# Kernel optimization log

Measured on AMD Instinct MI355X. Metric: run time of the kernel, lower is better.

## Reference

```python
import jax, jax.numpy as jnp
import numpy as np

B, N, D = 4, 2048, 1024
H, DH = 16, 64
SCALE = DH ** -0.5


def setup_inputs() -> dict:
    key = jax.random.key(0)
    k1, k2, k3 = jax.random.split(key, 3)
    z = jax.random.normal(k1, (B, N, D), dtype=jnp.float32)
    w_qkv = jax.random.normal(k2, (D, 3 * H * DH), dtype=jnp.float32) * (D ** -0.5)
    w_out = jax.random.normal(k3, (H * DH, D), dtype=jnp.float32) * ((H * DH) ** -0.5)
    b_out = jnp.zeros((D,), dtype=jnp.float32)
    return {"z": z, "w_qkv": w_qkv, "w_out": w_out, "b_out": b_out}


def reference(z, w_qkv, w_out, b_out):
    # qkv projection: (B,N,D) @ (D,3*H*DH) -> split into q,k,v
    qkv = z @ w_qkv  # (B, N, 3*H*DH)
    q, k, v = jnp.split(qkv, 3, axis=-1)
    # (B, N, H*DH) -> (B, H, N, DH)
    def heads(t):
        return t.reshape(B, N, H, DH).transpose(0, 2, 1, 3)
    q, k, v = heads(q), heads(k), heads(v)
    # scaled dot-product attention with full NxN scores (matches original)
    dots = jnp.einsum('bhid,bhjd->bhij', q, k) * SCALE
    attn = jax.nn.softmax(dots, axis=-1)
    out = jnp.einsum('bhij,bhjd->bhid', attn, v)  # (B, H, N, DH)
    out = out.transpose(0, 2, 1, 3).reshape(B, N, H * DH)
    return out @ w_out + b_out  # dropout is identity in eval
```

## Files before the change

kernel.cpp:

```cpp
#include <hip/hip_runtime.h>
#include <hip/hip_bf16.h>
#include <cstdint>
#include <cstddef>

typedef __attribute__((ext_vector_type(8))) short short8;
typedef __attribute__((ext_vector_type(4))) float f32x4;
typedef __attribute__((ext_vector_type(4))) unsigned uint4v;

#define LDS_AS __attribute__((address_space(3)))
#define GLB_AS __attribute__((address_space(1)))

__device__ __forceinline__ unsigned short f32_bf16(float f) {
  unsigned u = __builtin_bit_cast(unsigned, f);
  u += 0x7fffu + ((u >> 16) & 1u);
  return (unsigned short)(u >> 16);
}

__device__ __forceinline__ unsigned cvt_pk_bf16(float lo, float hi) {
  unsigned r;
  asm("v_cvt_pk_bf16_f32 %0, %1, %2" : "=v"(r) : "v"(lo), "v"(hi));
  return r;
}

__global__ __launch_bounds__(256) void k_cvt(const float* __restrict__ in,
                                             unsigned short* __restrict__ out, int n4) {
  int i = blockIdx.x * 256 + threadIdx.x;
  if (i >= n4) return;
  float4 v = reinterpret_cast<const float4*>(in)[i];
  ushort4 o;
  o.x = f32_bf16(v.x); o.y = f32_bf16(v.y); o.z = f32_bf16(v.z); o.w = f32_bf16(v.w);
  reinterpret_cast<ushort4*>(out)[i] = o;
}

__global__ __launch_bounds__(256) void k_cvt_t(const float* __restrict__ in,
                                               unsigned short* __restrict__ out,
                                               int R, int C) {
  __shared__ float t[32][33];
  int c0 = blockIdx.x * 32, r0 = blockIdx.y * 32;
  int lr = threadIdx.x & 31, lw = threadIdx.x >> 5;
#pragma unroll
  for (int i = 0; i < 32; i += 8)
    t[lw + i][lr] = in[(size_t)(r0 + lw + i) * C + c0 + lr];
  __syncthreads();
#pragma unroll
  for (int i = 0; i < 32; i += 8)
    out[(size_t)(c0 + lw + i) * R + r0 + lr] = f32_bf16(t[lr][lw + i]);
}

__device__ __forceinline__ void gemm_bt_mainloop(
    const unsigned short* __restrict__ A, const unsigned short* __restrict__ Bt,
    int K, int m0, int n0, unsigned short* lds, int tid, f32x4 acc[4][4]) {
  const int w = tid >> 6, l = tid & 63;
  const int wr = w >> 1, wc = w & 1;
  const int lr = l & 15, lg = l >> 4;
  unsigned short* As = lds;
  unsigned short* Bs = lds + 4096;
  for (int kt = 0; kt < K; kt += 32) {
    __syncthreads();
#pragma unroll
    for (int i = 0; i < 2; ++i) {
      int idx = i * 256 + tid;
      const unsigned short* g = A + (size_t)(m0 + (idx >> 2)) * K + kt + (idx & 3) * 8;
      __builtin_amdgcn_global_load_lds((const GLB_AS unsigned int*)g,
          (LDS_AS unsigned int*)(As + (size_t)(i * 256 + w * 64) * 8), 16, 0, 0);
    }
#pragma unroll
    for (int i = 0; i < 2; ++i) {
      int idx = i * 256 + tid;
      const unsigned short* g = Bt + (size_t)(n0 + (idx >> 2)) * K + kt + (idx & 3) * 8;
      __builtin_amdgcn_global_load_lds((const GLB_AS unsigned int*)g,
          (LDS_AS unsigned int*)(Bs + (size_t)(i * 256 + w * 64) * 8), 16, 0, 0);
    }
    __syncthreads();
    short8 a[4], b[4];
#pragma unroll
    for (int m = 0; m < 4; ++m)
      a[m] = *reinterpret_cast<const short8*>(As + (wr * 64 + m * 16 + lr) * 32 + lg * 8);
#pragma unroll
    for (int n = 0; n < 4; ++n)
      b[n] = *reinterpret_cast<const short8*>(Bs + (wc * 64 + n * 16 + lr) * 32 + lg * 8);
#pragma unroll
    for (int m = 0; m < 4; ++m)
#pragma unroll
      for (int n = 0; n < 4; ++n)
        acc[m][n] = __builtin_amdgcn_mfma_f32_16x16x32_bf16(a[m], b[n], acc[m][n], 0, 0, 0);
  }
}

__global__ __launch_bounds__(256) void k_gemm_qkv(
    const unsigned short* __restrict__ Zb, const unsigned short* __restrict__ Wt,
    unsigned short* __restrict__ Qb, unsigned short* __restrict__ Kb,
    unsigned short* __restrict__ Vt) {
  __shared__ unsigned short lds[8192];
  f32x4 acc[4][4];
#pragma unroll
  for (int m = 0; m < 4; ++m)
#pragma unroll
    for (int n = 0; n < 4; ++n) acc[m][n] = (f32x4){0.f, 0.f, 0.f, 0.f};
  const int m0 = blockIdx.x * 128, n0 = blockIdx.y * 128;
  gemm_bt_mainloop(Zb, Wt, 1024, m0, n0, lds, threadIdx.x, acc);
  const int tid = threadIdx.x, w = tid >> 6, l = tid & 63;
  const int wr = w >> 1, wc = w & 1, lr = l & 15, lg = l >> 4;
#pragma unroll
  for (int n = 0; n < 4; ++n) {
    int gc = n0 + wc * 64 + n * 16;
    int part = gc >> 10;
    int within = gc & 1023;
    int h = within >> 6;
    int dhb = (within & 63) + lr;
#pragma unroll
    for (int m = 0; m < 4; ++m) {
      int gr = m0 + wr * 64 + m * 16 + lg * 4;
      int b = gr >> 11, pos = gr & 2047;
      size_t bh = (size_t)(b * 16 + h);
      if (part == 0) {
        unsigned short* dst = Qb + bh * (2048 * 64) + (size_t)pos * 64 + dhb;
#pragma unroll
        for (int r = 0; r < 4; ++r) dst[r * 64] = f32_bf16(acc[m][n][r]);
      } else if (part == 1) {
        unsigned short* dst = Kb + bh * (2048 * 64) + (size_t)pos * 64 + dhb;
#pragma unroll
        for (int r = 0; r < 4; ++r) dst[r * 64] = f32_bf16(acc[m][n][r]);
      } else {
        unsigned short* dst = Vt + bh * (64 * 2048) + (size_t)dhb * 2048 + pos;
        ushort4 pv;
        pv.x = f32_bf16(acc[m][n][0]); pv.y = f32_bf16(acc[m][n][1]);
        pv.z = f32_bf16(acc[m][n][2]); pv.w = f32_bf16(acc[m][n][3]);
        *reinterpret_cast<ushort4*>(dst) = pv;
      }
    }
  }
}

__device__ __forceinline__ void softmax_pack(f32x4 s[4], float& m_r, float& l_r,
                                             f32x4 o[4], short8 pb[2], bool lgodd,
                                             float cc) {
  float t0 = fmaxf(fmaxf(s[0][0], s[0][1]), s[0][2]);
  float t1 = fmaxf(fmaxf(s[0][3], s[1][0]), s[1][1]);
  float t2 = fmaxf(fmaxf(s[1][2], s[1][3]), s[2][0]);
  float t3 = fmaxf(fmaxf(s[2][1], s[2][2]), s[2][3]);
  float t4 = fmaxf(fmaxf(s[3][0], s[3][1]), s[3][2]);
  float tl = fmaxf(fmaxf(fmaxf(t0, t1), fmaxf(t2, t3)), fmaxf(t4, s[3][3]));
  if (__any(tl > m_r + 8.0f)) {
    float tm = fmaxf(tl, __shfl_xor(tl, 16));
    tm = fmaxf(tm, __shfl_xor(tm, 32));
    float mn = fmaxf(m_r, tm);
    float al = __builtin_amdgcn_exp2f((m_r - mn) * cc);
    m_r = mn;
    l_r *= al;
#pragma unroll
    for (int c = 0; c < 4; ++c)
#pragma unroll
      for (int r = 0; r < 4; ++r) o[c][r] *= al;
  }
  float nb = m_r * cc;
  float rs = 0.f;
#pragma unroll
  for (int c = 0; c < 4; ++c)
#pragma unroll
    for (int r = 0; r < 4; ++r) {
      float p = __builtin_amdgcn_exp2f(s[c][r] * cc - nb);
      s[c][r] = p;
      rs += p;
    }
  rs += __shfl_xor(rs, 16);
  rs += __shfl_xor(rs, 32);
  l_r += rs;
  unsigned Ap[4], Bp[4];
#pragma unroll
  for (int c = 0; c < 4; ++c) {
    Ap[c] = cvt_pk_bf16(s[c][0], s[c][1]);
    Bp[c] = cvt_pk_bf16(s[c][2], s[c][3]);
  }
#pragma unroll
  for (int kc = 0; kc < 2; ++kc) {
    unsigned ua = Ap[2 * kc], va = Ap[2 * kc + 1];
    asm("v_permlane32_swap_b32 %0, %1" : "+v"(ua), "+v"(va));
    unsigned uas = (unsigned)__shfl_xor((int)ua, 16);
    unsigned vas = (unsigned)__shfl_xor((int)va, 16);
    unsigned w0 = lgodd ? vas : ua;
    unsigned w2 = lgodd ? va : uas;
    unsigned ub = Bp[2 * kc], vb = Bp[2 * kc + 1];
    asm("v_permlane32_swap_b32 %0, %1" : "+v"(ub), "+v"(vb));
    unsigned ubs = (unsigned)__shfl_xor((int)ub, 16);
    unsigned vbs = (unsigned)__shfl_xor((int)vb, 16);
    unsigned w1 = lgodd ? vbs : ub;
    unsigned w3 = lgodd ? vb : ubs;
    uint4v pw = (uint4v){w0, w1, w2, w3};
    pb[kc] = __builtin_bit_cast(short8, pw);
  }
}

__global__ __launch_bounds__(256, 4) void k_attn(
    const unsigned short* __restrict__ Q, const unsigned short* __restrict__ Kb,
    const unsigned short* __restrict__ Vt, unsigned short* __restrict__ O) {
  __shared__ unsigned short lds[16384];
  const int tid = threadIdx.x, w = tid >> 6, l = tid & 63;
  const int lr = l & 15, lg = l >> 4;
  const bool lgodd = (lg & 1) != 0;
  const int wg = blockIdx.x;
  const int xcd = wg & 7, local = wg >> 3;
  const int bh = xcd + ((local >> 4) << 3);
  const int qb = local & 15;
  const unsigned short* Qp = Q + (size_t)bh * (2048 * 64);
  const unsigned short* Kp = Kb + (size_t)bh * (2048 * 64);
  const unsigned short* Vp = Vt + (size_t)bh * (64 * 2048);
  const int q0 = qb * 128 + w * 32;

  short8 aq[2][2];
#pragma unroll
  for (int g = 0; g < 2; ++g)
#pragma unroll
    for (int kc = 0; kc < 2; ++kc)
      aq[g][kc] = *reinterpret_cast<const short8*>(
          Qp + (size_t)(q0 + g * 16 + lr) * 64 + kc * 32 + lg * 8);

  float m0r = -3e38f, l0r = 0.f, m1r = -3e38f, l1r = 0.f;
  f32x4 o0[4], o1[4];
#pragma unroll
  for (int c = 0; c < 4; ++c) {
    o0[c] = (f32x4){0.f, 0.f, 0.f, 0.f};
    o1[c] = (f32x4){0.f, 0.f, 0.f, 0.f};
  }
  const float cc = 0.125f * 1.44269504089f;

  const int srow = tid >> 3, sslot = tid & 7;
#define STAGE_KV(bufK, bufV, kv0)                                                     \
  {                                                                                   \
    _Pragma("unroll")                                                                 \
    for (int i = 0; i < 2; ++i) {                                                     \
      int row = i * 32 + srow;                                                        \
      int sw = sslot ^ (row & 7);                                                     \
      __builtin_amdgcn_global_load_lds(                                               \
          (const GLB_AS unsigned int*)(Kp + (size_t)((kv0) + row) * 64 + sw * 8),     \
          (LDS_AS unsigned int*)((bufK) + (i * 256 + tid) * 8), 16, 0, 0);            \
      __builtin_amdgcn_global_load_lds(                                               \
          (const GLB_AS unsigned int*)(Vp + (size_t)row * 2048 + (kv0) + sw * 8),     \
          (LDS_AS unsigned int*)((bufV) + (i * 256 + tid) * 8), 16, 0, 0);            \
    }                                                                                 \
  }

  unsigned short* K0 = lds;
  unsigned short* V0 = lds + 4096;
  unsigned short* K1 = lds + 8192;
  unsigned short* V1 = lds + 12288;

  STAGE_KV(K0, V0, 0);
  __syncthreads();

  for (int t = 0; t < 32; ++t) {
    unsigned short* Ks = (t & 1) ? K1 : K0;
    unsigned short* Vs = (t & 1) ? V1 : V0;
    if (t < 31) {
      unsigned short* Kn = (t & 1) ? K0 : K1;
      unsigned short* Vn = (t & 1) ? V0 : V1;
      STAGE_KV(Kn, Vn, (t + 1) * 64);
    }
    f32x4 s0[4], s1[4];
#pragma unroll
    for (int c = 0; c < 4; ++c) {
      s0[c] = (f32x4){0.f, 0.f, 0.f, 0.f};
      s1[c] = (f32x4){0.f, 0.f, 0.f, 0.f};
    }
#pragma unroll
    for (int c = 0; c < 4; ++c)
#pragma unroll
      for (int kc = 0; kc < 2; ++kc) {
        int row = c * 16 + lr;
        int sw = (kc * 4 + lg) ^ (row & 7);
        short8 ak = *reinterpret_cast<const short8*>(Ks + row * 64 + sw * 8);
        s0[c] = __builtin_amdgcn_mfma_f32_16x16x32_bf16(ak, aq[0][kc], s0[c], 0, 0, 0);
        s1[c] = __builtin_amdgcn_mfma_f32_16x16x32_bf16(ak, aq[1][kc], s1[c], 0, 0, 0);
      }
    short8 pb0[2], pb1[2];
    softmax_pack(s0, m0r, l0r, o0, pb0, lgodd, cc);
    softmax_pack(s1, m1r, l1r, o1, pb1, lgodd, cc);
#pragma unroll
    for (int c = 0; c < 4; ++c)
#pragma unroll
      for (int kc = 0; kc < 2; ++kc) {
        int row = c * 16 + lr;
        int sw = (kc * 4 + lg) ^ (row & 7);
        short8 av = *reinterpret_cast<const short8*>(Vs + row * 64 + sw * 8);
        o0[c] = __builtin_amdgcn_mfma_f32_16x16x32_bf16(av, pb0[kc], o0[c], 0, 0, 0);
        o1[c] = __builtin_amdgcn_mfma_f32_16x16x32_bf16(av, pb1[kc], o1[c], 0, 0, 0);
      }
    __syncthreads();
  }

  const int b = bh >> 4, h = bh & 15;
#pragma unroll
  for (int g = 0; g < 2; ++g) {
    const float inv = 1.0f / (g ? l1r : l0r);
    const f32x4* o = g ? o1 : o0;
    const size_t row = (size_t)b * 2048 + q0 + g * 16 + lr;
#pragma unroll
    for (int c = 0; c < 4; ++c) {
      ushort4 pv;
      pv.x = f32_bf16(o[c][0] * inv);
      pv.y = f32_bf16(o[c][1] * inv);
      pv.z = f32_bf16(o[c][2] * inv);
      pv.w = f32_bf16(o[c][3] * inv);
      *reinterpret_cast<ushort4*>(const_cast<unsigned short*>(
          O + row * 1024 + h * 64 + c * 16 + lg * 4)) = pv;
    }
  }
#undef STAGE_KV
}

__global__ __launch_bounds__(256) void k_gemm_out(
    const unsigned short* __restrict__ Ob, const unsigned short* __restrict__ Wt,
    const float* __restrict__ bias, float* __restrict__ out) {
  __shared__ unsigned short lds[8192];
  f32x4 acc[4][4];
#pragma unroll
  for (int m = 0; m < 4; ++m)
#pragma unroll
    for (int n = 0; n < 4; ++n) acc[m][n] = (f32x4){0.f, 0.f, 0.f, 0.f};
  const int m0 = blockIdx.x * 128, n0 = blockIdx.y * 128;
  gemm_bt_mainloop(Ob, Wt, 1024, m0, n0, lds, threadIdx.x, acc);
  const int tid = threadIdx.x, w = tid >> 6, l = tid & 63;
  const int wr = w >> 1, wc = w & 1, lr = l & 15, lg = l >> 4;
#pragma unroll
  for (int n = 0; n < 4; ++n) {
    int gc = n0 + wc * 64 + n * 16 + lr;
    float bo = bias[gc];
#pragma unroll
    for (int m = 0; m < 4; ++m) {
      int gr = m0 + wr * 64 + m * 16 + lg * 4;
#pragma unroll
      for (int r = 0; r < 4; ++r)
        out[(size_t)(gr + r) * 1024 + gc] = acc[m][n][r] + bo;
    }
  }
}

extern "C" void kernel_launch(void* const* d_in, const int* in_sizes, int n_in,
                              void* d_out, int out_size, void* d_ws, size_t ws_size,
                              hipStream_t stream) {
  const float* z     = (const float*)d_in[0];
  const float* w_qkv = (const float*)d_in[1];
  const float* w_out = (const float*)d_in[2];
  const float* b_out = (const float*)d_in[3];
  float* out = (float*)d_out;

  unsigned short* ws = (unsigned short*)d_ws;
  unsigned short* Zb    = ws;
  unsigned short* Wqkvt = ws + 8388608;
  unsigned short* Woutt = ws + 11534336;
  unsigned short* Qb    = ws + 12582912;
  unsigned short* Kb    = ws + 20971520;
  unsigned short* Vt    = ws + 29360128;
  unsigned short* Ob    = Zb;

  k_cvt<<<dim3(8192), dim3(256), 0, stream>>>(z, Zb, 2097152);
  k_cvt_t<<<dim3(96, 32), dim3(256), 0, stream>>>(w_qkv, Wqkvt, 1024, 3072);
  k_cvt_t<<<dim3(32, 32), dim3(256), 0, stream>>>(w_out, Woutt, 1024, 1024);
  k_gemm_qkv<<<dim3(64, 24), dim3(256), 0, stream>>>(Zb, Wqkvt, Qb, Kb, Vt);
  k_attn<<<dim3(1024), dim3(256), 0, stream>>>(Qb, Kb, Vt, Ob);
  k_gemm_out<<<dim3(64, 8), dim3(256), 0, stream>>>(Ob, Woutt, b_out, out);
}
```

Measured before the change: 213.1 us.

## Halve attention query tile per wave and double workgroup count

The attention kernel now gives each wave 16 query rows instead of 32, so each workgroup covers 64 queries and the grid grows to 2048 workgroups. Launch bounds rise to 5 waves per SIMD and the swizzle offsets are precomputed. The aim is lower register pressure and higher occupancy to hide latency. The cost is that every K/V tile staged in LDS is reused by half as many queries, which doubles global K/V traffic and the number of barriers per query.

```diff
diff --git a/kernel.cpp b/kernel.cpp
--- a/kernel.cpp
+++ b/kernel.cpp
@@ -191,7 +191,7 @@
   }
 }
 
-__global__ __launch_bounds__(256, 4) void k_attn(
+__global__ __launch_bounds__(256, 5) void k_attn(
     const unsigned short* __restrict__ Q, const unsigned short* __restrict__ Kb,
     const unsigned short* __restrict__ Vt, unsigned short* __restrict__ O) {
   __shared__ unsigned short lds[16384];
@@ -200,29 +200,28 @@
   const bool lgodd = (lg & 1) != 0;
   const int wg = blockIdx.x;
   const int xcd = wg & 7, local = wg >> 3;
-  const int bh = xcd + ((local >> 4) << 3);
-  const int qb = local & 15;
+  const int bh = xcd + ((local >> 5) << 3);
+  const int qb = local & 31;
   const unsigned short* Qp = Q + (size_t)bh * (2048 * 64);
   const unsigned short* Kp = Kb + (size_t)bh * (2048 * 64);
   const unsigned short* Vp = Vt + (size_t)bh * (64 * 2048);
-  const int q0 = qb * 128 + w * 32;
-
-  short8 aq[2][2];
-#pragma unroll
-  for (int g = 0; g < 2; ++g)
-#pragma unroll
-    for (int kc = 0; kc < 2; ++kc)
-      aq[g][kc] = *reinterpret_cast<const short8*>(
-          Qp + (size_t)(q0 + g * 16 + lr) * 64 + kc * 32 + lg * 8);
-
-  float m0r = -3e38f, l0r = 0.f, m1r = -3e38f, l1r = 0.f;
-  f32x4 o0[4], o1[4];
-#pragma unroll
-  for (int c = 0; c < 4; ++c) {
-    o0[c] = (f32x4){0.f, 0.f, 0.f, 0.f};
-    o1[c] = (f32x4){0.f, 0.f, 0.f, 0.f};
-  }
+  const int q0 = qb * 64 + w * 16;
+
+  short8 aq[2];
+#pragma unroll
+  for (int kc = 0; kc < 2; ++kc)
+    aq[kc] = *reinterpret_cast<const short8*>(
+        Qp + (size_t)(q0 + lr) * 64 + kc * 32 + lg * 8);
+
+  float m_r = -3e38f, l_r = 0.f;
+  f32x4 o[4];
+#pragma unroll
+  for (int c = 0; c < 4; ++c) o[c] = (f32x4){0.f, 0.f, 0.f, 0.f};
+  const f32x4 zero4 = (f32x4){0.f, 0.f, 0.f, 0.f};
   const float cc = 0.125f * 1.44269504089f;
+
+  const int sw0 = (lg ^ (lr & 7)) * 8;
+  const int sw1 = ((4 + lg) ^ (lr & 7)) * 8;
 
   const int srow = tid >> 3, sslot = tid & 7;
 #define STAGE_KV(bufK, bufV, kv0)                                                     \
@@ -256,54 +255,40 @@
       unsigned short* Vn = (t & 1) ? V0 : V1;
       STAGE_KV(Kn, Vn, (t + 1) * 64);
     }
-    f32x4 s0[4], s1[4];
+    f32x4 s[4];
 #pragma unroll
     for (int c = 0; c < 4; ++c) {
-      s0[c] = (f32x4){0.f, 0.f, 0.f, 0.f};
-      s1[c] = (f32x4){0.f, 0.f, 0.f, 0.f};
-    }
-#pragma unroll
-    for (int c = 0; c < 4; ++c)
-#pragma unroll
-      for (int kc = 0; kc < 2; ++kc) {
-        int row = c * 16 + lr;
-        int sw = (kc * 4 + lg) ^ (row & 7);
-        short8 ak = *reinterpret_cast<const short8*>(Ks + row * 64 + sw * 8);
-        s0[c] = __builtin_amdgcn_mfma_f32_16x16x32_bf16(ak, aq[0][kc], s0[c], 0, 0, 0);
-        s1[c] = __builtin_amdgcn_mfma_f32_16x16x32_bf16(ak, aq[1][kc], s1[c], 0, 0, 0);
-      }
-    short8 pb0[2], pb1[2];
-    softmax_pack(s0, m0r, l0r, o0, pb0, lgodd, cc);
-    softmax_pack(s1, m1r, l1r, o1, pb1, lgodd, cc);
-#pragma unroll
-    for (int c = 0; c < 4; ++c)
-#pragma unroll
-      for (int kc = 0; kc < 2; ++kc) {
-        int row = c * 16 + lr;
-        int sw = (kc * 4 + lg) ^ (row & 7);
-        short8 av = *reinterpret_cast<const short8*>(Vs + row * 64 + sw * 8);
-        o0[c] = __builtin_amdgcn_mfma_f32_16x16x32_bf16(av, pb0[kc], o0[c], 0, 0, 0);
-        o1[c] = __builtin_amdgcn_mfma_f32_16x16x32_bf16(av, pb1[kc], o1[c], 0, 0, 0);
-      }
+      const unsigned short* kb = Ks + c * 1024 + lr * 64;
+      short8 ak0 = *reinterpret_cast<const short8*>(kb + sw0);
+      short8 ak1 = *reinterpret_cast<const short8*>(kb + sw1);
+      s[c] = __builtin_amdgcn_mfma_f32_16x16x32_bf16(ak0, aq[0], zero4, 0, 0, 0);
+      s[c] = __builtin_amdgcn_mfma_f32_16x16x32_bf16(ak1, aq[1], s[c], 0, 0, 0);
+    }
+    short8 pb[2];
+    softmax_pack(s, m_r, l_r, o, pb, lgodd, cc);
+#pragma unroll
+    for (int c = 0; c < 4; ++c) {
+      const unsigned short* vb = Vs + c * 1024 + lr * 64;
+      short8 av0 = *reinterpret_cast<const short8*>(vb + sw0);
+      short8 av1 = *reinterpret_cast<const short8*>(vb + sw1);
+      o[c] = __builtin_amdgcn_mfma_f32_16x16x32_bf16(av0, pb[0], o[c], 0, 0, 0);
+      o[c] = __builtin_amdgcn_mfma_f32_16x16x32_bf16(av1, pb[1], o[c], 0, 0, 0);
+    }
     __syncthreads();
   }
 
   const int b = bh >> 4, h = bh & 15;
-#pragma unroll
-  for (int g = 0; g < 2; ++g) {
-    const float inv = 1.0f / (g ? l1r : l0r);
-    const f32x4* o = g ? o1 : o0;
-    const size_t row = (size_t)b * 2048 + q0 + g * 16 + lr;
-#pragma unroll
-    for (int c = 0; c < 4; ++c) {
-      ushort4 pv;
-      pv.x = f32_bf16(o[c][0] * inv);
-      pv.y = f32_bf16(o[c][1] * inv);
-      pv.z = f32_bf16(o[c][2] * inv);
-      pv.w = f32_bf16(o[c][3] * inv);
-      *reinterpret_cast<ushort4*>(const_cast<unsigned short*>(
-          O + row * 1024 + h * 64 + c * 16 + lg * 4)) = pv;
-    }
+  const float inv = 1.0f / l_r;
+  const size_t row = (size_t)b * 2048 + q0 + lr;
+#pragma unroll
+  for (int c = 0; c < 4; ++c) {
+    ushort4 pv;
+    pv.x = f32_bf16(o[c][0] * inv);
+    pv.y = f32_bf16(o[c][1] * inv);
+    pv.z = f32_bf16(o[c][2] * inv);
+    pv.w = f32_bf16(o[c][3] * inv);
+    *reinterpret_cast<ushort4*>(
+        const_cast<unsigned short*>(O + row * 1024 + h * 64 + c * 16 + lg * 4)) = pv;
   }
 #undef STAGE_KV
 }
@@ -357,6 +342,6 @@
   k_cvt_t<<<dim3(96, 32), dim3(256), 0, stream>>>(w_qkv, Wqkvt, 1024, 3072);
   k_cvt_t<<<dim3(32, 32), dim3(256), 0, stream>>>(w_out, Woutt, 1024, 1024);
   k_gemm_qkv<<<dim3(64, 24), dim3(256), 0, stream>>>(Zb, Wqkvt, Qb, Kb, Vt);
-  k_attn<<<dim3(1024), dim3(256), 0, stream>>>(Qb, Kb, Vt, Ob);
+  k_attn<<<dim3(2048), dim3(256), 0, stream>>>(Qb, Kb, Vt, Ob);
   k_gemm_out<<<dim3(64, 8), dim3(256), 0, stream>>>(Ob, Woutt, b_out, out);
 }
```

After: 230.3 us. 1.08x slower.
